# Performance work log

Hardware: AMD Instinct MI355X
Metric: run time of the kernel (lower is better)

Reference implementation:

```python
import jax, jax.numpy as jnp
import numpy as np

N, M = 50000, 32
F_NODE, F_EDGE = 64, 64


def setup_inputs() -> dict:
    key = jax.random.key(0)
    k1, k2, k3, k4, k5 = jax.random.split(key, 5)
    node_in_fea = jax.random.normal(k1, (N, F_NODE), dtype=jnp.float32)
    edge_fea = jax.random.normal(k2, (N, M, F_EDGE), dtype=jnp.float32)
    # indices in [-1, N); -1 marks invalid neighbor (masked out), as in the torch code
    edge_fea_idx = jax.random.randint(k3, (N, M), -1, N)
    # fc_full: Linear(2*F_NODE + F_EDGE -> 2*F_NODE), kaiming-uniform-ish init
    fan_in = 2 * F_NODE + F_EDGE
    bound = float(np.sqrt(6.0 / fan_in))
    W = jax.random.uniform(k4, (2 * F_NODE, fan_in), minval=-bound, maxval=bound, dtype=jnp.float32)
    b = jnp.zeros((2 * F_NODE,), dtype=jnp.float32)
    alpha = jnp.float32(0.7)
    return {"node_in_fea": node_in_fea, "edge_fea": edge_fea,
            "edge_fea_idx": edge_fea_idx, "W": W, "b": b, "alpha": alpha}


def softplus(x):
    return jax.nn.softplus(x)


def reference(node_in_fea, edge_fea, edge_fea_idx, W, b, alpha):
    n, m = edge_fea_idx.shape
    # gather neighbor node features; clip -1 -> 0 (result is masked to zero below,
    # matching torch where idx=-1 wraps but contribution is zeroed by the mask)
    safe_idx = jnp.clip(edge_fea_idx, 0)
    node_edge_fea = node_in_fea[safe_idx]                       # (N, M, F)
    self_fea = jnp.broadcast_to(node_in_fea[:, None, :], (n, m, node_in_fea.shape[-1]))
    total_nbr_fea = jnp.concatenate([self_fea, node_edge_fea, edge_fea], axis=2)  # (N, M, 2F+Fe)
    total_gated_fea = jnp.einsum('nmf,of->nmo', total_nbr_fea, W) + b             # (N, M, 2F)
    nbr_filter, nbr_core = jnp.split(total_gated_fea, 2, axis=2)
    mask = (edge_fea_idx >= 0).astype(nbr_filter.dtype)[:, :, None]
    nbr_filter = jax.nn.sigmoid(nbr_filter) * mask
    nbr_core = softplus(nbr_core) * mask
    nbr_sumed = jnp.sum(nbr_filter * nbr_core, axis=1)          # (N, F)
    out = softplus(alpha * node_in_fea + nbr_sumed)
    return out
```

## Files before the change

### kernel.cpp

```cpp
#include <hip/hip_runtime.h>
#include <hip/hip_bf16.h>

#define MNBR 32
#define FDIM 64

typedef __attribute__((ext_vector_type(8))) short bf16x8;
typedef __attribute__((ext_vector_type(16))) float f32x16;
typedef __attribute__((ext_vector_type(4))) float f32x4;
typedef __attribute__((ext_vector_type(4))) float fvec4;

static __device__ __forceinline__ unsigned short f2bf(float x) {
    unsigned u = __builtin_bit_cast(unsigned, x);
    u += 0x7FFFu + ((u >> 16) & 1u);
    return (unsigned short)(u >> 16);
}
static __device__ __forceinline__ bf16x8 pack8(fvec4 a, fvec4 b) {
    bf16x8 r;
    r[0] = (short)f2bf(a[0]); r[1] = (short)f2bf(a[1]);
    r[2] = (short)f2bf(a[2]); r[3] = (short)f2bf(a[3]);
    r[4] = (short)f2bf(b[0]); r[5] = (short)f2bf(b[1]);
    r[6] = (short)f2bf(b[2]); r[7] = (short)f2bf(b[3]);
    return r;
}
static __device__ __forceinline__ float sigmoid_f(float x) {
    return __builtin_amdgcn_rcpf(1.f + __expf(-x));
}
static __device__ __forceinline__ float softplus_f(float x) {
    return fmaxf(x, 0.f) + __logf(1.f + __expf(-fabsf(x)));
}

__global__ __launch_bounds__(256) void prep_kernel(
    const float* __restrict__ node, const float* __restrict__ W,
    const float* __restrict__ b, float* __restrict__ A_pk,
    short* __restrict__ nodeBF, short* __restrict__ Wfrag, int n_nodes)
{
    const int lane = threadIdx.x & 63;
    const int w    = threadIdx.x >> 6;
    const int c = lane & 15, g = lane >> 4;

    if (blockIdx.x == 0) {
        const int c32 = lane & 31, hi = lane >> 5;
        for (int fi = w; fi < 32; fi += 4) {
            int t = fi >> 3, s = fi & 7;
            int o = t * 32 + c32;
            int kcol = (s < 4) ? (128 + s * 16 + hi * 8)
                               : (64 + (s - 4) * 16 + hi * 8);
            const float* wp = W + (size_t)o * 192 + kcol;
            bf16x8 fr;
            #pragma unroll
            for (int j = 0; j < 8; ++j) fr[j] = (short)f2bf(wp[j]);
            *(bf16x8*)(Wfrag + ((size_t)fi * 64 + lane) * 8) = fr;
        }
    }

    bf16x8 Wsf[8][2];
    float bias[8];
    #pragma unroll
    for (int t = 0; t < 8; ++t) {
        const int o = t * 16 + c;
        bias[t] = b[o];
        #pragma unroll
        for (int s = 0; s < 2; ++s) {
            const float* wp = W + (size_t)o * 192 + s * 32 + g * 8;
            fvec4 w0 = *(const fvec4*)(wp);
            fvec4 w1 = *(const fvec4*)(wp + 4);
            Wsf[t][s] = pack8(w0, w1);
        }
    }

    const int ntiles = (n_nodes + 15) >> 4;
    for (int rt = blockIdx.x * 4 + w; rt < ntiles; rt += gridDim.x * 4) {
        const int row = rt * 16 + c;
        const float* p = node + (size_t)row * FDIM + g * 8;
        fvec4 e0 = *(const fvec4*)(p);
        fvec4 e1 = *(const fvec4*)(p + 4);
        fvec4 e2 = *(const fvec4*)(p + 32);
        fvec4 e3 = *(const fvec4*)(p + 36);
        bf16x8 af0 = pack8(e0, e1);
        bf16x8 af1 = pack8(e2, e3);
        *(bf16x8*)(nodeBF + (size_t)row * FDIM + g * 8)      = af0;
        *(bf16x8*)(nodeBF + (size_t)row * FDIM + 32 + g * 8) = af1;

        f32x4 acc[8];
        #pragma unroll
        for (int t = 0; t < 8; ++t) acc[t] = (f32x4){0.f, 0.f, 0.f, 0.f};
        #pragma unroll
        for (int t = 0; t < 8; ++t) {
            acc[t] = __builtin_amdgcn_mfma_f32_16x16x32_bf16(af0, Wsf[t][0], acc[t], 0, 0, 0);
            acc[t] = __builtin_amdgcn_mfma_f32_16x16x32_bf16(af1, Wsf[t][1], acc[t], 0, 0, 0);
        }
        #pragma unroll
        for (int t = 0; t < 8; ++t) {
            const int o = t * 16 + c;
            const size_t base = ((size_t)(o & 31)) * 4 + (o >> 5);
            #pragma unroll
            for (int r = 0; r < 4; ++r) {
                int n = rt * 16 + g * 4 + r;
                A_pk[(size_t)n * 128 + base] = acc[t][r] + bias[t];
            }
        }
    }
}

__global__ __launch_bounds__(256) void edge_fused(
    const float* __restrict__ node, const float* __restrict__ edge,
    const int* __restrict__ eidx, const float* __restrict__ A_pk,
    const short* __restrict__ nodeBF, const short* __restrict__ Wfrag,
    const float* __restrict__ alphap, float* __restrict__ out, int n_nodes)
{
    __shared__ short sW[32 * 64 * 8];
    for (int i = threadIdx.x; i < 32 * 64; i += 256)
        *(bf16x8*)(sW + (size_t)i * 8) = *(const bf16x8*)(Wfrag + (size_t)i * 8);
    __syncthreads();

    const int lane = threadIdx.x & 63;
    const int w    = threadIdx.x >> 6;
    const int c32 = lane & 31, hi = lane >> 5;
    const float alpha = alphap[0];

    for (int n = blockIdx.x * 4 + w; n < n_nodes; n += gridDim.x * 4) {
        const int j = eidx[(size_t)n * MNBR + c32];
        const int jsafe = (j < 0) ? 0 : j;

        const fvec4 aq = *(const fvec4*)(A_pk + (size_t)n * 128 + c32 * 4);
        const float ns = node[(size_t)n * FDIM + lane];

        const float* ep = edge + ((size_t)n * MNBR + c32) * FDIM + hi * 8;
        bf16x8 ea[4];
        #pragma unroll
        for (int s = 0; s < 4; ++s) {
            fvec4 x0 = __builtin_nontemporal_load((const fvec4*)(ep + s * 16));
            fvec4 x1 = __builtin_nontemporal_load((const fvec4*)(ep + s * 16 + 4));
            ea[s] = pack8(x0, x1);
        }
        const short* np_ = nodeBF + (size_t)jsafe * FDIM + hi * 8;
        bf16x8 na[4];
        #pragma unroll
        for (int s = 0; s < 4; ++s)
            na[s] = *(const bf16x8*)(np_ + s * 16);

        f32x16 acc[4] = {};
        #pragma unroll
        for (int s = 0; s < 8; ++s) {
            const bf16x8 afr = (s < 4) ? ea[s] : na[s - 4];
            #pragma unroll
            for (int t = 0; t < 4; ++t) {
                bf16x8 wf = *(const bf16x8*)(sW + ((size_t)(t * 8 + s) * 64 + lane) * 8);
                acc[t] = __builtin_amdgcn_mfma_f32_32x32x16_bf16(afr, wf, acc[t], 0, 0, 0);
            }
        }

        float nsum0 = 0.f, nsum1 = 0.f;
        #pragma unroll
        for (int r = 0; r < 16; ++r) {
            const int row = (r & 3) + 8 * (r >> 2) + 4 * hi;
            const int jr = __shfl(j, row, 32);
            const float m = (jr >= 0) ? 1.f : 0.f;
            float gf0 = acc[0][r] + aq[0], gc0 = acc[2][r] + aq[2];
            float gf1 = acc[1][r] + aq[1], gc1 = acc[3][r] + aq[3];
            nsum0 += m * (sigmoid_f(gf0) * softplus_f(gc0));
            nsum1 += m * (sigmoid_f(gf1) * softplus_f(gc1));
        }
        nsum0 += __shfl_xor(nsum0, 32);
        nsum1 += __shfl_xor(nsum1, 32);
        const float v = hi ? nsum1 : nsum0;
        out[(size_t)n * FDIM + lane] = softplus_f(fmaf(alpha, ns, v));
    }
}

extern "C" void kernel_launch(void* const* d_in, const int* in_sizes, int n_in,
                              void* d_out, int out_size, void* d_ws, size_t ws_size,
                              hipStream_t stream) {
    const float* node  = (const float*)d_in[0];
    const float* edge  = (const float*)d_in[1];
    const int*   eidx  = (const int*)d_in[2];
    const float* W     = (const float*)d_in[3];
    const float* b     = (const float*)d_in[4];
    const float* alpha = (const float*)d_in[5];
    float* out = (float*)d_out;

    const int n_nodes = in_sizes[0] / FDIM;

    char* ws = (char*)d_ws;
    short* nodeBF = (short*)ws;
    float* A_pk   = (float*)(ws + (size_t)n_nodes * FDIM * 2);
    short* Wfrag  = (short*)(ws + (size_t)n_nodes * FDIM * 2
                                + (size_t)n_nodes * 128 * 4);

    const int ntiles = (n_nodes + 15) >> 4;
    prep_kernel<<<(ntiles + 3) / 4, 256, 0, stream>>>(node, W, b, A_pk, nodeBF,
                                                      Wfrag, n_nodes);
    edge_fused<<<2048, 256, 0, stream>>>(node, edge, eidx, A_pk, nodeBF, Wfrag,
                                         alpha, out, n_nodes);
}
```

Measured before the change: 781.0 us.

## Software-pipeline edge kernel loads across nodes with double-buffered operand registers

Restructures the per-wave node loop into a two-stage software pipeline. The edge-feature, neighbor-feature, A_pk and index loads for the next node are issued before the current node's MFMA and activation work, and indices are prefetched two nodes ahead. The aim is to hide global-memory latency behind compute. The neighbor mask becomes a ballot bitmask instead of per-row shuffles, and launch bounds request 2 blocks per CU. Holding two operand sets raises register pressure, which could limit occupancy or cause spills.

```diff
diff --git a/kernel.cpp b/kernel.cpp
--- a/kernel.cpp
+++ b/kernel.cpp
@@ -102,7 +102,15 @@
     }
 }
 
-__global__ __launch_bounds__(256) void edge_fused(
+struct Ops {
+    fvec4 raw[8];
+    bf16x8 na[4];
+    fvec4 aq;
+    float ns;
+    unsigned long long mv;
+};
+
+__global__ __launch_bounds__(256, 2) void edge_fused(
     const float* __restrict__ node, const float* __restrict__ edge,
     const int* __restrict__ eidx, const float* __restrict__ A_pk,
     const short* __restrict__ nodeBF, const short* __restrict__ Wfrag,
@@ -118,31 +126,33 @@
     const int c32 = lane & 31, hi = lane >> 5;
     const float alpha = alphap[0];
 
-    for (int n = blockIdx.x * 4 + w; n < n_nodes; n += gridDim.x * 4) {
-        const int j = eidx[(size_t)n * MNBR + c32];
+    auto loadOps = [&](int n, int j, Ops& O) {
+        O.mv = __ballot(j >= 0);
         const int jsafe = (j < 0) ? 0 : j;
-
-        const fvec4 aq = *(const fvec4*)(A_pk + (size_t)n * 128 + c32 * 4);
-        const float ns = node[(size_t)n * FDIM + lane];
-
+        O.aq = *(const fvec4*)(A_pk + (size_t)n * 128 + c32 * 4);
+        O.ns = node[(size_t)n * FDIM + lane];
         const float* ep = edge + ((size_t)n * MNBR + c32) * FDIM + hi * 8;
+        #pragma unroll
+        for (int s = 0; s < 4; ++s) {
+            O.raw[2 * s]     = __builtin_nontemporal_load((const fvec4*)(ep + s * 16));
+            O.raw[2 * s + 1] = __builtin_nontemporal_load((const fvec4*)(ep + s * 16 + 4));
+        }
+        const short* np_ = nodeBF + (size_t)jsafe * FDIM + hi * 8;
+        #pragma unroll
+        for (int s = 0; s < 4; ++s)
+            O.na[s] = *(const bf16x8*)(np_ + s * 16);
+    };
+
+    auto computeNode = [&](int n, Ops& O) {
         bf16x8 ea[4];
         #pragma unroll
-        for (int s = 0; s < 4; ++s) {
-            fvec4 x0 = __builtin_nontemporal_load((const fvec4*)(ep + s * 16));
-            fvec4 x1 = __builtin_nontemporal_load((const fvec4*)(ep + s * 16 + 4));
-            ea[s] = pack8(x0, x1);
-        }
-        const short* np_ = nodeBF + (size_t)jsafe * FDIM + hi * 8;
-        bf16x8 na[4];
-        #pragma unroll
         for (int s = 0; s < 4; ++s)
-            na[s] = *(const bf16x8*)(np_ + s * 16);
+            ea[s] = pack8(O.raw[2 * s], O.raw[2 * s + 1]);
 
         f32x16 acc[4] = {};
         #pragma unroll
         for (int s = 0; s < 8; ++s) {
-            const bf16x8 afr = (s < 4) ? ea[s] : na[s - 4];
+            const bf16x8 afr = (s < 4) ? ea[s] : O.na[s - 4];
             #pragma unroll
             for (int t = 0; t < 4; ++t) {
                 bf16x8 wf = *(const bf16x8*)(sW + ((size_t)(t * 8 + s) * 64 + lane) * 8);
@@ -154,17 +164,42 @@
         #pragma unroll
         for (int r = 0; r < 16; ++r) {
             const int row = (r & 3) + 8 * (r >> 2) + 4 * hi;
-            const int jr = __shfl(j, row, 32);
-            const float m = (jr >= 0) ? 1.f : 0.f;
-            float gf0 = acc[0][r] + aq[0], gc0 = acc[2][r] + aq[2];
-            float gf1 = acc[1][r] + aq[1], gc1 = acc[3][r] + aq[3];
+            const float m = ((O.mv >> row) & 1ull) ? 1.f : 0.f;
+            float gf0 = acc[0][r] + O.aq[0], gc0 = acc[2][r] + O.aq[2];
+            float gf1 = acc[1][r] + O.aq[1], gc1 = acc[3][r] + O.aq[3];
             nsum0 += m * (sigmoid_f(gf0) * softplus_f(gc0));
             nsum1 += m * (sigmoid_f(gf1) * softplus_f(gc1));
         }
         nsum0 += __shfl_xor(nsum0, 32);
         nsum1 += __shfl_xor(nsum1, 32);
         const float v = hi ? nsum1 : nsum0;
-        out[(size_t)n * FDIM + lane] = softplus_f(fmaf(alpha, ns, v));
+        out[(size_t)n * FDIM + lane] = softplus_f(fmaf(alpha, O.ns, v));
+    };
+
+    const int nstride = gridDim.x * 4;
+    int n1 = blockIdx.x * 4 + w;
+    int j1 = eidx[(size_t)n1 * MNBR + c32];
+    int n2 = n1 + nstride;
+    int j2 = (n2 < n_nodes) ? eidx[(size_t)n2 * MNBR + c32] : -1;
+
+    Ops A, B;
+    loadOps(n1, j1, A);
+
+    for (;;) {
+        int n3 = n2 + nstride;
+        int j3 = (n3 < n_nodes) ? eidx[(size_t)n3 * MNBR + c32] : -1;
+        if (n2 < n_nodes) loadOps(n2, j2, B);
+        computeNode(n1, A);
+        if (n2 >= n_nodes) break;
+
+        int n4 = n3 + nstride;
+        int j4 = (n4 < n_nodes) ? eidx[(size_t)n4 * MNBR + c32] : -1;
+        if (n3 < n_nodes) loadOps(n3, j3, A);
+        computeNode(n2, B);
+        if (n3 >= n_nodes) break;
+
+        n1 = n3;
+        n2 = n4; j2 = j4;
     }
 }
 
```

Result: slower. 842.4 us (+7.9%).
